# Performance work log

Measured on AMD Instinct MI355X. Metric: run time of the kernel, lower is better.

Reference implementation:

```python
import jax, jax.numpy as jnp
import numpy as np

B = 2
SPATIAL = (480, 360, 32)  # cylindrical grid (rho, phi, z) as in Cylinder3D
N = 400000
C = 32
EPS = 1e-5
NEG_SLOPE = 0.01
OFFSETS = [(d0, d2) for d0 in (-1, 0, 1) for d2 in (-1, 0, 1)]  # kernel (3,1,3)


def setup_inputs() -> dict:
    key = jax.random.key(0)
    k1, k2 = jax.random.split(key)
    # unique active voxel coordinates: sample unique linear indices then decode
    total = B * SPATIAL[0] * SPATIAL[1] * SPATIAL[2]
    rng = np.random.default_rng(0)
    lin = rng.choice(total, size=N, replace=False).astype(np.int64)
    b = lin // (SPATIAL[0] * SPATIAL[1] * SPATIAL[2])
    r = lin % (SPATIAL[0] * SPATIAL[1] * SPATIAL[2])
    c0 = r // (SPATIAL[1] * SPATIAL[2])
    r = r % (SPATIAL[1] * SPATIAL[2])
    c1 = r // SPATIAL[2]
    c2 = r % SPATIAL[2]
    coords = jnp.asarray(np.stack([b, c0, c1, c2], axis=1), dtype=jnp.int32)
    features = jax.random.normal(k1, (N, C), dtype=jnp.float32)
    weight = jax.random.normal(k2, (9, C, C), dtype=jnp.float32) * (1.0 / np.sqrt(9 * C))
    gamma = jnp.ones((C,), dtype=jnp.float32)
    beta = jnp.zeros((C,), dtype=jnp.float32)
    return {"features": features, "coords": coords, "weight": weight,
            "gamma": gamma, "beta": beta}


def _subm_conv(features, coords, weight):
    n = features.shape[0]
    # dense coordinate -> row-index lookup table (rulebook hash)
    lookup = jnp.full((B,) + SPATIAL, -1, dtype=jnp.int32)
    lookup = lookup.at[coords[:, 0], coords[:, 1], coords[:, 2], coords[:, 3]].set(
        jnp.arange(n, dtype=jnp.int32))
    out = jnp.zeros((n, weight.shape[-1]), dtype=features.dtype)
    for k, (d0, d2) in enumerate(OFFSETS):
        n0 = coords[:, 1] + d0
        n2 = coords[:, 3] + d2
        valid = (n0 >= 0) & (n0 < SPATIAL[0]) & (n2 >= 0) & (n2 < SPATIAL[2])
        nbr = lookup[coords[:, 0],
                     jnp.clip(n0, 0, SPATIAL[0] - 1),
                     coords[:, 2],
                     jnp.clip(n2, 0, SPATIAL[2] - 1)]
        nbr = jnp.where(valid, nbr, -1)
        # gather (masked) -> GEMM -> accumulate (scatter to same active sites)
        gathered = jnp.where((nbr >= 0)[:, None],
                             features[jnp.clip(nbr, 0)], 0.0)
        out = out + gathered @ weight[k]
    return out


def reference(features, coords, weight, gamma, beta):
    x = _subm_conv(features, coords, weight)          # [N, C]
    x = jnp.where(x >= 0, x, NEG_SLOPE * x)           # LeakyReLU (before BN per forward)
    mean = jnp.mean(x, axis=0)                        # BatchNorm1d, training mode
    var = jnp.mean((x - mean) ** 2, axis=0)           # biased variance
    y = (x - mean) * jax.lax.rsqrt(var + EPS) * gamma + beta
    return y
```

## Files before the change

### kernel.cpp

```cpp
#include <hip/hip_runtime.h>
#include <hip/hip_bf16.h>

#define S0 480
#define S1 360
#define S2 32
#define SLAB (S1 * S2)
#define CH 32
#define EPS 1e-5f
#define SLOPE 0.01f

#define NCOL (2 * S0 * S1)
#define SCAN_BLKS (NCOL / 256)

typedef short short8 __attribute__((ext_vector_type(8)));
typedef float f32x16 __attribute__((ext_vector_type(16)));

__device__ __forceinline__ unsigned short f2b(float f) {
    union { __hip_bfloat16 b; unsigned short u; } v;
    v.b = __float2bfloat16(f);
    return v.u;
}

__global__ __launch_bounds__(256) void clear_mask_k(uint4* __restrict__ mask)
{
    int i = blockIdx.x * 256 + threadIdx.x;
    if (i < NCOL / 4) mask[i] = make_uint4(0u, 0u, 0u, 0u);
}

__global__ __launch_bounds__(256) void scatter_or_k(
    const int4* __restrict__ coords, unsigned int* __restrict__ mask, int n)
{
    int i = blockIdx.x * 256 + threadIdx.x;
    if (i < n) {
        int4 c = coords[i];
        int col = (c.x * S0 + c.y) * S1 + c.z;
        atomicOr(&mask[col], 1u << c.w);
    }
}

__global__ __launch_bounds__(256) void scanA_k(
    const unsigned int* __restrict__ mask, int* __restrict__ bsum,
    const float* __restrict__ weight, short8* __restrict__ bfrag)
{
    int t = threadIdx.x;
    int pc = __popc(mask[blockIdx.x * 256 + t]);
#pragma unroll
    for (int m = 32; m > 0; m >>= 1) pc += __shfl_xor(pc, m, 64);
    __shared__ int red[4];
    if ((t & 63) == 0) red[t >> 6] = pc;
    __syncthreads();
    if (t == 0) bsum[blockIdx.x] = red[0] + red[1] + red[2] + red[3];

    if (blockIdx.x == 0 && t < 64) {
        int half = t >> 5;
        int col  = t & 31;
#pragma unroll
        for (int k = 0; k < 9; ++k)
#pragma unroll
            for (int h = 0; h < 2; ++h) {
                short8 fr;
#pragma unroll
                for (int j = 0; j < 8; ++j) {
                    int ic = h * 16 + half * 8 + j;
                    fr[j] = (short)f2b(weight[k * (CH * CH) + ic * CH + col]);
                }
                bfrag[(k * 2 + h) * 64 + t] = fr;
            }
    }
}

__global__ __launch_bounds__(256) void scanBC_k(
    const unsigned int* __restrict__ mask, const int* __restrict__ bsum,
    uint2* __restrict__ tab)
{
    int t = threadIdx.x;
    int b = blockIdx.x;

    int partial = 0;
    for (int j = t; j < b; j += 256) partial += bsum[j];
#pragma unroll
    for (int m = 32; m > 0; m >>= 1) partial += __shfl_xor(partial, m, 64);
    __shared__ int red[4];
    if ((t & 63) == 0) red[t >> 6] = partial;
    __syncthreads();
    int base = red[0] + red[1] + red[2] + red[3];

    int col = b * 256 + t;
    unsigned int m = mask[col];
    int pc = __popc(m);
    __shared__ int sa[256], sb[256];
    sa[t] = pc; __syncthreads();
    int* src = sa; int* dst = sb;
#pragma unroll
    for (int off = 1; off < 256; off <<= 1) {
        dst[t] = src[t] + (t >= off ? src[t - off] : 0);
        __syncthreads();
        int* tmp = src; src = dst; dst = tmp;
    }
    int excl = src[t] - pc + base;
    tab[col] = make_uint2(m, (unsigned int)excl);
}

__global__ __launch_bounds__(256) void rank_k(
    const int4*  __restrict__ coords,
    const uint2* __restrict__ tab,
    uint2*       __restrict__ pinfo,
    int*         __restrict__ rankof,
    int n)
{
    int i = blockIdx.x * 256 + threadIdx.x;
    if (i >= n) return;
    int4 c = coords[i];
    int col = (c.x * S0 + c.y) * S1 + c.z;
    int lin = col * 32 + c.w;
    uint2 tv = tab[col];
    int rank = (int)tv.y + __popc(tv.x & ((1u << c.w) - 1u));
    pinfo[rank] = make_uint2((unsigned int)i, (unsigned int)lin);
    rankof[i] = rank;
}

__global__ __launch_bounds__(256) void pack_k(
    const float* __restrict__ features,
    const uint2* __restrict__ pinfo,
    unsigned short* __restrict__ featb,
    int n, int ntile)
{
    int NB  = gridDim.x;
    int bpx = NB >> 3;
    int xcd = blockIdx.x & 7;
    int ibx = blockIdx.x >> 3;
    int chunk = (ntile + 7) >> 3;
    int rstart = xcd * chunk * 32;
    int rend   = min((xcd + 1) * chunk, ntile) * 32;
    if (rend > n) rend = n;

    int t = threadIdx.x;
    int j = t & 7;
    int sub = t >> 3;
    for (int row = rstart + ibx * 32 + sub; row < rend; row += bpx * 32) {
        unsigned int orig = pinfo[row].x;
        float4 f = ((const float4*)(features + (size_t)orig * CH))[j];
        ushort4 u;
        u.x = f2b(f.x); u.y = f2b(f.y); u.z = f2b(f.z); u.w = f2b(f.w);
        ((ushort4*)(featb + (size_t)row * CH))[j] = u;
    }
}

__global__ __launch_bounds__(256) void conv_sorted_k(
    const unsigned short* __restrict__ featb,
    const uint2* __restrict__ pinfo,
    const uint2* __restrict__ tab,
    const short8* __restrict__ bfrag,
    unsigned short* __restrict__ xout,
    float*        __restrict__ stats_part,
    int n, int ntile)
{
    int tid  = threadIdx.x;
    int lane = tid & 63;
    int wv   = tid >> 6;
    int half = lane >> 5;
    int col  = lane & 31;

    short8 B[9][2];
#pragma unroll
    for (int t = 0; t < 9; ++t) {
        B[t][0] = bfrag[(t * 2 + 0) * 64 + lane];
        B[t][1] = bfrag[(t * 2 + 1) * 64 + lane];
    }

    int NB  = gridDim.x;
    int bpx = NB >> 3;
    int xcd = blockIdx.x & 7;
    int ibx = blockIdx.x >> 3;
    int chunk = (ntile + 7) >> 3;
    int wpx = bpx * 4;
    int run = (chunk + wpx - 1) / wpx;
    int wix = ibx * 4 + wv;
    int xend = min((xcd + 1) * chunk, ntile);
    int t0 = xcd * chunk + wix * run;
    int t1 = min(t0 + run, xend);

    float s = 0.f, qq = 0.f;

    for (int tile = t0; tile < t1; ++tile) {
        int p = tile * 32 + col;
        bool live = (p < n);
        int pc = live ? p : 0;

        uint2 pi = pinfo[pc];
        int lin = (int)pi.y;
        int c2 = lin & 31;
        int colv = lin >> 5;
        int c0 = (lin / SLAB) % S0;

        int nbr[9];
#pragma unroll
        for (int d0 = 0; d0 < 3; ++d0) {
            int n0 = c0 + d0 - 1;
            bool v0 = (n0 >= 0) & (n0 < S0) & live;
            uint2 tv = v0 ? tab[colv + (d0 - 1) * S1] : make_uint2(0u, 0u);
#pragma unroll
            for (int d2 = 0; d2 < 3; ++d2) {
                int n2 = c2 + d2 - 1;
                int rk = -1;
                if (v0 && n2 >= 0 && n2 < S2 && ((tv.x >> n2) & 1u))
                    rk = (int)tv.y + __popc(tv.x & ((1u << n2) - 1u));
                nbr[d0 * 3 + d2] = rk;
            }
        }

        bool act[9];
#pragma unroll
        for (int t = 0; t < 9; ++t) act[t] = (__any(nbr[t] >= 0) != 0);

        short8 A0[9], A1[9];
#pragma unroll
        for (int t = 0; t < 9; ++t) {
            short8 z;
#pragma unroll
            for (int j = 0; j < 8; ++j) z[j] = 0;
            A0[t] = z; A1[t] = z;
            int nb = nbr[t];
            if (nb >= 0) {
                const short* fp = (const short*)featb + (size_t)nb * CH;
                A0[t] = *(const short8*)(fp + half * 8);
                A1[t] = *(const short8*)(fp + 16 + half * 8);
            }
        }

        f32x16 acc;
#pragma unroll
        for (int i = 0; i < 16; ++i) acc[i] = 0.f;
#pragma unroll
        for (int t = 0; t < 9; ++t) {
            if (act[t]) {
                acc = __builtin_amdgcn_mfma_f32_32x32x16_bf16(A0[t], B[t][0], acc, 0, 0, 0);
                acc = __builtin_amdgcn_mfma_f32_32x32x16_bf16(A1[t], B[t][1], acc, 0, 0, 0);
            }
        }

#pragma unroll
        for (int i = 0; i < 16; ++i) {
            float v = acc[i];
            v = v >= 0.f ? v : SLOPE * v;
            int row = (i & 3) + 8 * (i >> 2) + 4 * half;
            int prow = tile * 32 + row;
            if (prow < n) {
                xout[(size_t)prow * CH + col] = f2b(v);
                s += v; qq += v * v;
            }
        }
    }

    s  += __shfl_xor(s, 32);
    qq += __shfl_xor(qq, 32);

    __shared__ float lsum[4][32];
    __shared__ float lsq[4][32];
    if (lane < 32) { lsum[wv][col] = s; lsq[wv][col] = qq; }
    __syncthreads();
    if (tid < 32) {
        stats_part[(size_t)blockIdx.x * 64 + tid] =
            lsum[0][tid] + lsum[1][tid] + lsum[2][tid] + lsum[3][tid];
    } else if (tid < 64) {
        int cc = tid - 32;
        stats_part[(size_t)blockIdx.x * 64 + tid] =
            lsq[0][cc] + lsq[1][cc] + lsq[2][cc] + lsq[3][cc];
    }
}

__global__ __launch_bounds__(256) void reduce_stats_k(
    const float* __restrict__ part, float* __restrict__ stats, int nb)
{
    int c = blockIdx.x;
    float s = 0.f;
    for (int i = threadIdx.x; i < nb; i += 256)
        s += part[(size_t)i * 64 + c];
#pragma unroll
    for (int m = 32; m > 0; m >>= 1) s += __shfl_xor(s, m, 64);
    __shared__ float red[4];
    int wv = threadIdx.x >> 6;
    if ((threadIdx.x & 63) == 0) red[wv] = s;
    __syncthreads();
    if (threadIdx.x == 0) stats[c] = red[0] + red[1] + red[2] + red[3];
}

__global__ __launch_bounds__(256) void bn_gather_k(
    const unsigned short* __restrict__ xb,
    const int*   __restrict__ rankof,
    const float* __restrict__ stats,
    const float* __restrict__ gamma,
    const float* __restrict__ beta,
    float* __restrict__ out,
    int n)
{
    int total = n * 4;
    int stride = gridDim.x * blockDim.x;
    int g = blockIdx.x * blockDim.x + threadIdx.x;
    int c8 = g & 3;

    float scale[8], shift[8];
    float rn = 1.0f / (float)n;
#pragma unroll
    for (int j = 0; j < 8; ++j) {
        int oc = c8 * 8 + j;
        float m  = stats[oc] * rn;
        float vv = stats[CH + oc] * rn - m * m;
        float iv = rsqrtf(vv + EPS) * gamma[oc];
        scale[j] = iv;
        shift[j] = beta[oc] - m * iv;
    }

    const short8* x8 = (const short8*)xb;
    for (; g < total; g += stride) {
        int i = g >> 2;
        int rank = rankof[i];
        short8 v = x8[(size_t)rank * 4 + c8];
        float f[8];
#pragma unroll
        for (int j = 0; j < 8; ++j) {
            union { unsigned int u; float f; } w;
            w.u = ((unsigned int)(unsigned short)v[j]) << 16;
            f[j] = fmaf(w.f, scale[j], shift[j]);
        }
        float4* o = (float4*)(out + (size_t)i * CH + c8 * 8);
        o[0] = make_float4(f[0], f[1], f[2], f[3]);
        o[1] = make_float4(f[4], f[5], f[6], f[7]);
    }
}

extern "C" void kernel_launch(void* const* d_in, const int* in_sizes, int n_in,
                              void* d_out, int out_size, void* d_ws, size_t ws_size,
                              hipStream_t stream)
{
    const float* features = (const float*)d_in[0];
    const int4*  coords   = (const int4*)d_in[1];
    const float* weight   = (const float*)d_in[2];
    const float* gamma    = (const float*)d_in[3];
    const float* beta     = (const float*)d_in[4];
    float* out = (float*)d_out;

    int n = in_sizes[0] / CH;
    int ntile = (n + 31) / 32;
    int conv_blocks = 2048;

    char* w = (char*)d_ws;
    unsigned int* mask = (unsigned int*)w;  w += (size_t)NCOL * 4;
    uint2* tab = (uint2*)w;                 w += (size_t)NCOL * 8;
    int* bsum = (int*)w;                    w += ((size_t)SCAN_BLKS * 4 + 255) & ~(size_t)255;
    uint2* pinfo = (uint2*)w;               w += (size_t)n * 8;
    int* rankof = (int*)w;                  w += (size_t)n * 4;
    unsigned short* featb = (unsigned short*)w; w += (size_t)n * CH * 2;
    unsigned short* xout = (unsigned short*)w;  w += (size_t)n * CH * 2;
    float* stats_part = (float*)w;          w += (size_t)conv_blocks * 64 * 4;
    short8* bfrag = (short8*)w;             w += 9 * 2 * 64 * sizeof(short8);
    float* stats = (float*)w;

    clear_mask_k<<<(NCOL / 4 + 255) / 256, 256, 0, stream>>>((uint4*)mask);
    scatter_or_k<<<(n + 255) / 256, 256, 0, stream>>>(coords, mask, n);
    scanA_k<<<SCAN_BLKS, 256, 0, stream>>>(mask, bsum, weight, bfrag);
    scanBC_k<<<SCAN_BLKS, 256, 0, stream>>>(mask, bsum, tab);
    rank_k<<<(n + 255) / 256, 256, 0, stream>>>(coords, tab, pinfo, rankof, n);
    pack_k<<<2048, 256, 0, stream>>>(features, pinfo, featb, n, ntile);

    conv_sorted_k<<<conv_blocks, 256, 0, stream>>>(
        featb, pinfo, tab, bfrag, xout, stats_part, n, ntile);

    reduce_stats_k<<<64, 256, 0, stream>>>(stats_part, stats, conv_blocks);

    bn_gather_k<<<2048, 256, 0, stream>>>(xout, rankof, stats, gamma, beta, out, n);
}
```

Before: 110.3 us.

## Give each conv wave one tile and make neighbor gathers branchless via zero row

```diff
diff --git a/kernel.cpp b/kernel.cpp
--- a/kernel.cpp
+++ b/kernel.cpp
@@ -21,10 +21,13 @@
     return v.u;
 }
 
-__global__ __launch_bounds__(256) void clear_mask_k(uint4* __restrict__ mask)
+__global__ __launch_bounds__(256) void clear_k(uint4* __restrict__ mask,
+                                               uint4* __restrict__ zrow)
 {
     int i = blockIdx.x * 256 + threadIdx.x;
     if (i < NCOL / 4) mask[i] = make_uint4(0u, 0u, 0u, 0u);
+    if (blockIdx.x == 0 && threadIdx.x < 4)
+        zrow[threadIdx.x] = make_uint4(0u, 0u, 0u, 0u);
 }
 
 __global__ __launch_bounds__(256) void scatter_or_k(
@@ -146,7 +149,7 @@
     }
 }
 
-__global__ __launch_bounds__(256) void conv_sorted_k(
+__global__ __launch_bounds__(256, 2) void conv_sorted_k(
     const unsigned short* __restrict__ featb,
     const uint2* __restrict__ pinfo,
     const uint2* __restrict__ tab,
@@ -168,21 +171,16 @@
         B[t][1] = bfrag[(t * 2 + 1) * 64 + lane];
     }
 
-    int NB  = gridDim.x;
-    int bpx = NB >> 3;
     int xcd = blockIdx.x & 7;
     int ibx = blockIdx.x >> 3;
     int chunk = (ntile + 7) >> 3;
-    int wpx = bpx * 4;
-    int run = (chunk + wpx - 1) / wpx;
-    int wix = ibx * 4 + wv;
-    int xend = min((xcd + 1) * chunk, ntile);
-    int t0 = xcd * chunk + wix * run;
-    int t1 = min(t0 + run, xend);
+    int idx = ibx * 4 + wv;
+    int tile = xcd * chunk + idx;
+    bool tlive = (idx < chunk) && (tile < ntile);
 
     float s = 0.f, qq = 0.f;
 
-    for (int tile = t0; tile < t1; ++tile) {
+    if (tlive) {
         int p = tile * 32 + col;
         bool live = (p < n);
         int pc = live ? p : 0;
@@ -198,14 +196,15 @@
         for (int d0 = 0; d0 < 3; ++d0) {
             int n0 = c0 + d0 - 1;
             bool v0 = (n0 >= 0) & (n0 < S0) & live;
-            uint2 tv = v0 ? tab[colv + (d0 - 1) * S1] : make_uint2(0u, 0u);
+            int cidx = colv + (d0 - 1) * S1;
+            cidx = min(max(cidx, 0), NCOL - 1);
+            uint2 tv = tab[cidx];
 #pragma unroll
             for (int d2 = 0; d2 < 3; ++d2) {
                 int n2 = c2 + d2 - 1;
-                int rk = -1;
-                if (v0 && n2 >= 0 && n2 < S2 && ((tv.x >> n2) & 1u))
-                    rk = (int)tv.y + __popc(tv.x & ((1u << n2) - 1u));
-                nbr[d0 * 3 + d2] = rk;
+                bool hit = v0 & (n2 >= 0) & (n2 < S2) & (((tv.x >> (n2 & 31)) & 1u) != 0);
+                int rk = (int)tv.y + __popc(tv.x & ((1u << (n2 & 31)) - 1u));
+                nbr[d0 * 3 + d2] = hit ? rk : -1;
             }
         }
 
@@ -216,16 +215,10 @@
         short8 A0[9], A1[9];
 #pragma unroll
         for (int t = 0; t < 9; ++t) {
-            short8 z;
-#pragma unroll
-            for (int j = 0; j < 8; ++j) z[j] = 0;
-            A0[t] = z; A1[t] = z;
-            int nb = nbr[t];
-            if (nb >= 0) {
-                const short* fp = (const short*)featb + (size_t)nb * CH;
-                A0[t] = *(const short8*)(fp + half * 8);
-                A1[t] = *(const short8*)(fp + 16 + half * 8);
-            }
+            int nbc = nbr[t] >= 0 ? nbr[t] : n;
+            const short* fp = (const short*)featb + (size_t)nbc * CH;
+            A0[t] = *(const short8*)(fp + half * 8);
+            A1[t] = *(const short8*)(fp + 16 + half * 8);
         }
 
         f32x16 acc;
@@ -342,7 +335,8 @@
 
     int n = in_sizes[0] / CH;
     int ntile = (n + 31) / 32;
-    int conv_blocks = 2048;
+    int chunk = (ntile + 7) / 8;
+    int conv_blocks = 8 * ((chunk + 3) / 4);
 
     char* w = (char*)d_ws;
     unsigned int* mask = (unsigned int*)w;  w += (size_t)NCOL * 4;
@@ -350,13 +344,14 @@
     int* bsum = (int*)w;                    w += ((size_t)SCAN_BLKS * 4 + 255) & ~(size_t)255;
     uint2* pinfo = (uint2*)w;               w += (size_t)n * 8;
     int* rankof = (int*)w;                  w += (size_t)n * 4;
-    unsigned short* featb = (unsigned short*)w; w += (size_t)n * CH * 2;
+    unsigned short* featb = (unsigned short*)w; w += (size_t)(n + 4) * CH * 2;
     unsigned short* xout = (unsigned short*)w;  w += (size_t)n * CH * 2;
     float* stats_part = (float*)w;          w += (size_t)conv_blocks * 64 * 4;
     short8* bfrag = (short8*)w;             w += 9 * 2 * 64 * sizeof(short8);
     float* stats = (float*)w;
 
-    clear_mask_k<<<(NCOL / 4 + 255) / 256, 256, 0, stream>>>((uint4*)mask);
+    clear_k<<<(NCOL / 4 + 255) / 256, 256, 0, stream>>>(
+        (uint4*)mask, (uint4*)(featb + (size_t)n * CH));
     scatter_or_k<<<(n + 255) / 256, 256, 0, stream>>>(coords, mask, n);
     scanA_k<<<SCAN_BLKS, 256, 0, stream>>>(mask, bsum, weight, bfrag);
     scanBC_k<<<SCAN_BLKS, 256, 0, stream>>>(mask, bsum, tab);
```

Result: faster. 104.3 us (-5.4%).
